# Kernel tuning notes

Measured on AMD Instinct MI355X. Metric: run time of the kernel, lower is better.

The kernel has to match this reference:

```python
import jax, jax.numpy as jnp
import numpy as np

N_CONS, N_VARS, N_EDGES, N_CAND = 100000, 200000, 8000000, 20000
C_FEAT, V_FEAT = 5, 19


def setup_inputs() -> dict:
    key = jax.random.key(0)
    k1, k2, k3, k4, k5, k6 = jax.random.split(key, 6)
    constraint = jax.random.normal(k1, (N_CONS, C_FEAT), dtype=jnp.float32)
    variable = jax.random.normal(k2, (N_VARS, V_FEAT), dtype=jnp.float32)
    c_edge_index = jax.random.randint(k3, (N_EDGES,), 0, N_CONS, dtype=jnp.int64)
    v_edge_index = jax.random.randint(k4, (N_EDGES,), 0, N_VARS, dtype=jnp.int64)
    cv_edge_index = jnp.stack([c_edge_index, v_edge_index], axis=0)  # [2, E]
    edge_attr = jax.random.normal(k5, (N_EDGES,), dtype=jnp.float32)
    cand_mask = jax.random.randint(k6, (N_CAND,), 0, N_VARS, dtype=jnp.int64)
    return {
        "constraint": constraint,
        "variable": variable,
        "cv_edge_index": cv_edge_index,
        "edge_attr": edge_attr,
        "cand_mask": cand_mask,
    }


def reference(constraint, variable, cv_edge_index, edge_attr, cand_mask):
    # Expression encoded in from_expression:
    #   variable_1_5   = variable[:, 5][v_edge_index]       (gather var feat to edges)
    #   constraint_1_2 = constraint[:, 2][c_edge_index]     (gather cons feat to edges)
    #   msg   = variable_1_5 * edge_attr + constraint_1_2   (edge elementwise)
    #   agg   = scatter_sum(msg, v_edge_index, n_vars)      (scatter to variables)
    #   res   = agg * variable[:, 0] + sqrt(abs(variable[:, 3]))
    #   return res[cand_mask]
    c_edge_index = cv_edge_index[0]
    v_edge_index = cv_edge_index[1]
    variable_1_5 = variable[:, 5][v_edge_index]      # [E]
    constraint_1_2 = constraint[:, 2][c_edge_index]  # [E]
    msg = variable_1_5 * edge_attr + constraint_1_2  # [E]
    agg = jax.ops.segment_sum(msg, v_edge_index, num_segments=variable.shape[0])  # [n_vars]
    result = agg * variable[:, 0] + jnp.sqrt(jnp.abs(variable[:, 3]))
    return result[cand_mask]
```

## Files before the change

### kernel.cpp

```cpp
#include <hip/hip_runtime.h>
#include <math.h>

#define N_CONS  100000
#define N_VARS  200000
#define N_EDGES 8000000
#define N_CAND  20000
#define C_FEAT  5
#define V_FEAT  19
#define BM_WORDS      6250
#define BM_WORDS_PAD  6400
#define ACC_SLOTS     20000
#define CMP_BLOCKS    512
#define WAVES_TOTAL   (CMP_BLOCKS * 1024 / 64)
#define REGION_STRIDE 1024
#define ACC_BLOCKS    128
#define REGIONS_PER_BLOCK (WAVES_TOTAL / ACC_BLOCKS)
#define CID_BLOCKS    ((ACC_SLOTS + 255) / 256)

__global__ void pack_kernel(const float* __restrict__ variable,
                            const float* __restrict__ constraint,
                            const int* __restrict__ cand,
                            float* __restrict__ var5,
                            float* __restrict__ cons2,
                            unsigned int* __restrict__ bitmap) {
    int i = blockIdx.x * blockDim.x + threadIdx.x;
    if (i < N_VARS) var5[i]  = variable[i * V_FEAT + 5];
    if (i < N_CONS) cons2[i] = constraint[i * C_FEAT + 2];
    if (i < N_CAND) {
        int v = cand[i];
        atomicOr(&bitmap[v >> 5], 1u << (v & 31));
    }
}

__global__ void __launch_bounds__(1024)
scan_kernel(const unsigned int* __restrict__ bitmap,
            uint2* __restrict__ bp) {
    __shared__ unsigned int wsum[16];
    const int CH = 7;
    int t = threadIdx.x;
    int lane = t & 63, wid = t >> 6;
    int base = t * CH;
    unsigned int w_loc[CH];
    unsigned int pf_loc[CH];
    unsigned int sum = 0;
#pragma unroll
    for (int j = 0; j < CH; ++j) {
        int w = base + j;
        unsigned int word = (w < BM_WORDS_PAD) ? bitmap[w] : 0u;
        w_loc[j]  = word;
        pf_loc[j] = sum;
        sum += __popc(word);
    }
    unsigned int inc = sum;
#pragma unroll
    for (int off = 1; off < 64; off <<= 1) {
        unsigned int n = __shfl_up(inc, off, 64);
        if (lane >= off) inc += n;
    }
    if (lane == 63) wsum[wid] = inc;
    __syncthreads();
    if (wid == 0 && lane < 16) {
        unsigned int v = wsum[lane];
#pragma unroll
        for (int off = 1; off < 16; off <<= 1) {
            unsigned int n = __shfl_up(v, off, 16);
            if (lane >= off) v += n;
        }
        wsum[lane] = v;
    }
    __syncthreads();
    unsigned int ebase = inc - sum + (wid ? wsum[wid - 1] : 0u);
#pragma unroll
    for (int j = 0; j < CH; ++j) {
        int w = base + j;
        if (w < BM_WORDS_PAD) bp[w] = make_uint2(w_loc[j], ebase + pf_loc[j]);
    }
}

__global__ void __launch_bounds__(1024, 8)
compact_kernel(const int* __restrict__ c_idx,
               const int* __restrict__ v_idx,
               const float* __restrict__ edge_attr,
               const float* __restrict__ var5,
               const float* __restrict__ cons2,
               const uint2* __restrict__ bp,
               uint2* __restrict__ recs,
               int* __restrict__ wcount) {
    __shared__ uint2 lds_bp[BM_WORDS_PAD];
    {
        const uint4* src = (const uint4*)bp;
        uint4* dst = (uint4*)lds_bp;
        for (int j = threadIdx.x; j < BM_WORDS_PAD / 2; j += blockDim.x)
            dst[j] = src[j];
    }
    __syncthreads();

    const int nch = N_EDGES / 4;
    const int stride = gridDim.x * blockDim.x;
    const int lane = threadIdx.x & 63;
    const unsigned long long lt = (1ull << lane) - 1ull;
    const int wgid = (blockIdx.x * blockDim.x + threadIdx.x) >> 6;
    uint2* region = recs + (size_t)wgid * REGION_STRIDE;
    int woff = 0;

    for (int g = blockIdx.x * blockDim.x + threadIdx.x; g < nch; g += stride) {
        int4   v = ((const int4*)v_idx)[g];
        int4   c = ((const int4*)c_idx)[g];
        float4 e = ((const float4*)edge_attr)[g];

#define SLOT(vv, cc, ee)                                                     \
        {                                                                    \
            uint2 e2 = lds_bp[(vv) >> 5];                                    \
            bool keep = (e2.x >> ((vv) & 31)) & 1u;                          \
            unsigned long long m = __ballot(keep);                           \
            if (keep) {                                                      \
                int cid = (int)e2.y +                                        \
                          __popc(e2.x & ((1u << ((vv) & 31)) - 1u));         \
                float msg = var5[vv] * (ee) + cons2[cc];                     \
                region[woff + __popcll(m & lt)] =                            \
                    make_uint2((unsigned)cid, __float_as_uint(msg));         \
            }                                                                \
            woff += __popcll(m);                                             \
        }
        SLOT(v.x, c.x, e.x)  SLOT(v.y, c.y, e.y)
        SLOT(v.z, c.z, e.z)  SLOT(v.w, c.w, e.w)
#undef SLOT
    }
    if (lane == 0) wcount[wgid] = woff;
}

__global__ void __launch_bounds__(1024, 4)
accum_kernel(const uint2* __restrict__ recs,
             const int* __restrict__ wcount,
             float* __restrict__ partials) {
    __shared__ float acc[ACC_SLOTS];
    for (int j = threadIdx.x; j < ACC_SLOTS; j += 1024) acc[j] = 0.0f;
    __syncthreads();

    int sub = threadIdx.x >> 7;
    int idx = threadIdx.x & 127;
    for (int rr = 0; rr < REGIONS_PER_BLOCK; rr += 8) {
        int r = blockIdx.x * REGIONS_PER_BLOCK + rr + sub;
        int cnt = wcount[r];
        const uint2* region = recs + (size_t)r * REGION_STRIDE;
        for (int i = idx; i < cnt; i += 128) {
            uint2 rec = region[i];
            atomicAdd(&acc[rec.x], __uint_as_float(rec.y));
        }
    }
    __syncthreads();

    float4* dst = (float4*)(partials + (size_t)blockIdx.x * ACC_SLOTS);
    const float4* src = (const float4*)acc;
    for (int j = threadIdx.x; j < ACC_SLOTS / 4; j += 1024)
        dst[j] = src[j];
}

__global__ void reduce_kernel(const float* __restrict__ partials,
                              float* __restrict__ agg2) {
    int cid = blockIdx.x * 256 + threadIdx.x;
    if (cid >= ACC_SLOTS) return;
    float s = 0.0f;
#pragma unroll 8
    for (int k = 0; k < ACC_BLOCKS; ++k)
        s += partials[(size_t)k * ACC_SLOTS + cid];
    agg2[cid] = s;
}

__global__ void out_kernel(const int* __restrict__ cand,
                           const float* __restrict__ agg2,
                           const uint2* __restrict__ bp,
                           const float* __restrict__ variable,
                           float* __restrict__ out) {
    int i = blockIdx.x * blockDim.x + threadIdx.x;
    if (i >= N_CAND) return;
    int v = cand[i];
    uint2 e2 = bp[v >> 5];
    int cid = (int)e2.y + __popc(e2.x & ((1u << (v & 31)) - 1u));
    out[i] = agg2[cid] * variable[v * V_FEAT + 0] + sqrtf(fabsf(variable[v * V_FEAT + 3]));
}

extern "C" void kernel_launch(void* const* d_in, const int* in_sizes, int n_in,
                              void* d_out, int out_size, void* d_ws, size_t ws_size,
                              hipStream_t stream) {
    const float* constraint = (const float*)d_in[0];
    const float* variable   = (const float*)d_in[1];
    const int*   cv_edge    = (const int*)d_in[2];
    const float* edge_attr  = (const float*)d_in[3];
    const int*   cand_mask  = (const int*)d_in[4];
    float* out = (float*)d_out;

    const int* c_idx = cv_edge;
    const int* v_idx = cv_edge + N_EDGES;

    float* var5  = (float*)d_ws;
    float* cons2 = var5 + N_VARS;
    unsigned int* bitmap = (unsigned int*)(cons2 + N_CONS);
    uint2* bp            = (uint2*)(bitmap + BM_WORDS_PAD);
    int*   wcount        = (int*)(bp + BM_WORDS_PAD);
    float* agg2          = (float*)(wcount + WAVES_TOTAL);
    float* partials      = agg2 + ACC_SLOTS;
    uint2* recs          = (uint2*)(partials + (size_t)ACC_BLOCKS * ACC_SLOTS);

    hipMemsetAsync(bitmap, 0, BM_WORDS_PAD * sizeof(unsigned int), stream);

    {
        int threads = 256;
        int blocks = (N_VARS + threads - 1) / threads;
        pack_kernel<<<blocks, threads, 0, stream>>>(variable, constraint, cand_mask,
                                                    var5, cons2, bitmap);
    }
    scan_kernel<<<1, 1024, 0, stream>>>(bitmap, bp);
    compact_kernel<<<CMP_BLOCKS, 1024, 0, stream>>>(c_idx, v_idx, edge_attr,
                                                    var5, cons2, bp, recs, wcount);
    accum_kernel<<<ACC_BLOCKS, 1024, 0, stream>>>(recs, wcount, partials);
    reduce_kernel<<<CID_BLOCKS, 256, 0, stream>>>(partials, agg2);
    {
        int threads = 256;
        int blocks = (N_CAND + threads - 1) / threads;
        out_kernel<<<blocks, threads, 0, stream>>>(cand_mask, agg2, bp, variable, out);
    }
}
```

Measured before the change: 66.33 us.

## Split edge compaction into index-only filter and gather-on-accumulate

The compaction kernel now streams only the variable-index array and writes (edge id, compacted slot) records. The edge message (var5*edge_attr + cons2) is computed later in the accumulate kernel by gathering c_idx, edge_attr, v_idx and the feature arrays for kept edges only. The aim is to cut the bulk streaming traffic of the filter pass. The cost is dependent random gathers in the accumulate stage, and at roughly 10% keep density most cache lines of those arrays are likely touched anyway. Region stride is halved with an overflow guard, and the accumulate grid is doubled, which doubles the partial buffers that the reduce pass must sum.

```diff
diff --git a/kernel.cpp b/kernel.cpp
--- a/kernel.cpp
+++ b/kernel.cpp
@@ -12,8 +12,8 @@
 #define ACC_SLOTS     20000
 #define CMP_BLOCKS    512
 #define WAVES_TOTAL   (CMP_BLOCKS * 1024 / 64)
-#define REGION_STRIDE 1024
-#define ACC_BLOCKS    128
+#define REGION_STRIDE 512
+#define ACC_BLOCKS    256
 #define REGIONS_PER_BLOCK (WAVES_TOTAL / ACC_BLOCKS)
 #define CID_BLOCKS    ((ACC_SLOTS + 255) / 256)
 
@@ -78,14 +78,10 @@
 }
 
 __global__ void __launch_bounds__(1024, 8)
-compact_kernel(const int* __restrict__ c_idx,
-               const int* __restrict__ v_idx,
-               const float* __restrict__ edge_attr,
-               const float* __restrict__ var5,
-               const float* __restrict__ cons2,
-               const uint2* __restrict__ bp,
-               uint2* __restrict__ recs,
-               int* __restrict__ wcount) {
+filter_kernel(const int* __restrict__ v_idx,
+              const uint2* __restrict__ bp,
+              uint2* __restrict__ recs,
+              int* __restrict__ wcount) {
     __shared__ uint2 lds_bp[BM_WORDS_PAD];
     {
         const uint4* src = (const uint4*)bp;
@@ -104,11 +100,10 @@
     int woff = 0;
 
     for (int g = blockIdx.x * blockDim.x + threadIdx.x; g < nch; g += stride) {
-        int4   v = ((const int4*)v_idx)[g];
-        int4   c = ((const int4*)c_idx)[g];
-        float4 e = ((const float4*)edge_attr)[g];
-
-#define SLOT(vv, cc, ee)                                                     \
+        int4 v = ((const int4*)v_idx)[g];
+        int eid0 = 4 * g;
+
+#define SLOT(vv, ee)                                                         \
         {                                                                    \
             uint2 e2 = lds_bp[(vv) >> 5];                                    \
             bool keep = (e2.x >> ((vv) & 31)) & 1u;                          \
@@ -116,21 +111,26 @@
             if (keep) {                                                      \
                 int cid = (int)e2.y +                                        \
                           __popc(e2.x & ((1u << ((vv) & 31)) - 1u));         \
-                float msg = var5[vv] * (ee) + cons2[cc];                     \
-                region[woff + __popcll(m & lt)] =                            \
-                    make_uint2((unsigned)cid, __float_as_uint(msg));         \
+                int slot = woff + __popcll(m & lt);                          \
+                if (slot < REGION_STRIDE)                                    \
+                    region[slot] = make_uint2((unsigned)(ee), (unsigned)cid);\
             }                                                                \
             woff += __popcll(m);                                             \
         }
-        SLOT(v.x, c.x, e.x)  SLOT(v.y, c.y, e.y)
-        SLOT(v.z, c.z, e.z)  SLOT(v.w, c.w, e.w)
+        SLOT(v.x, eid0 + 0)  SLOT(v.y, eid0 + 1)
+        SLOT(v.z, eid0 + 2)  SLOT(v.w, eid0 + 3)
 #undef SLOT
     }
     if (lane == 0) wcount[wgid] = woff;
 }
 
 __global__ void __launch_bounds__(1024, 4)
-accum_kernel(const uint2* __restrict__ recs,
+accum_kernel(const int* __restrict__ v_idx,
+             const int* __restrict__ c_idx,
+             const float* __restrict__ edge_attr,
+             const float* __restrict__ var5,
+             const float* __restrict__ cons2,
+             const uint2* __restrict__ recs,
              const int* __restrict__ wcount,
              float* __restrict__ partials) {
     __shared__ float acc[ACC_SLOTS];
@@ -142,10 +142,14 @@
     for (int rr = 0; rr < REGIONS_PER_BLOCK; rr += 8) {
         int r = blockIdx.x * REGIONS_PER_BLOCK + rr + sub;
         int cnt = wcount[r];
+        if (cnt > REGION_STRIDE) cnt = REGION_STRIDE;
         const uint2* region = recs + (size_t)r * REGION_STRIDE;
         for (int i = idx; i < cnt; i += 128) {
             uint2 rec = region[i];
-            atomicAdd(&acc[rec.x], __uint_as_float(rec.y));
+            int eid = (int)rec.x;
+            int v = v_idx[eid];
+            float msg = var5[v] * edge_attr[eid] + cons2[c_idx[eid]];
+            atomicAdd(&acc[rec.y], msg);
         }
     }
     __syncthreads();
@@ -211,9 +215,10 @@
                                                     var5, cons2, bitmap);
     }
     scan_kernel<<<1, 1024, 0, stream>>>(bitmap, bp);
-    compact_kernel<<<CMP_BLOCKS, 1024, 0, stream>>>(c_idx, v_idx, edge_attr,
-                                                    var5, cons2, bp, recs, wcount);
-    accum_kernel<<<ACC_BLOCKS, 1024, 0, stream>>>(recs, wcount, partials);
+    filter_kernel<<<CMP_BLOCKS, 1024, 0, stream>>>(v_idx, bp, recs, wcount);
+    accum_kernel<<<ACC_BLOCKS, 1024, 0, stream>>>(v_idx, c_idx, edge_attr,
+                                                  var5, cons2, recs, wcount,
+                                                  partials);
     reduce_kernel<<<CID_BLOCKS, 256, 0, stream>>>(partials, agg2);
     {
         int threads = 256;
```

Result: slower. 68.92 us (+3.9%).
